# Kernel tuning notes

Measured on AMD Instinct MI355X. Metric: run time of the kernel, lower is better.

Reference implementation:

```python
import jax, jax.numpy as jnp
import numpy as np

B = 8192
NV = 778   # MANO vertices
NJ = 16    # LBS joints
PARENTS = np.array([0, 0, 1, 2, 0, 4, 5, 0, 7, 8, 0, 10, 11, 0, 13, 14])


def quat2mat(quat):
    # quat: [N,4] (w,x,y,z) -> [N,3,3]
    q = quat / jnp.linalg.norm(quat, axis=1, keepdims=True)
    w, x, y, z = q[:, 0], q[:, 1], q[:, 2], q[:, 3]
    w2, x2, y2, z2 = w * w, x * x, y * y, z * z
    wx, wy, wz = w * x, w * y, w * z
    xy, xz, yz = x * y, x * z, y * z
    R = jnp.stack([
        w2 + x2 - y2 - z2, 2 * xy - 2 * wz, 2 * wy + 2 * xz,
        2 * wz + 2 * xy, w2 - x2 + y2 - z2, 2 * yz - 2 * wx,
        2 * xz - 2 * wy, 2 * wx + 2 * yz, w2 - x2 - y2 + z2,
    ], axis=1)
    return R.reshape(-1, 3, 3)


def batch_rodrigues(theta):
    # theta: [N,3] axis-angle -> [N,3,3]
    angle = jnp.linalg.norm(theta + 1e-8, axis=1, keepdims=True)
    normalized = theta / angle
    half = angle * 0.5
    quat = jnp.concatenate([jnp.cos(half), jnp.sin(half) * normalized], axis=1)
    return quat2mat(quat)


def qmul(q, r):
    # Hamilton product, (w,x,y,z); q,r: [N,4]
    w1, x1, y1, z1 = q[:, 0], q[:, 1], q[:, 2], q[:, 3]
    w2, x2, y2, z2 = r[:, 0], r[:, 1], r[:, 2], r[:, 3]
    return jnp.stack([
        w1 * w2 - x1 * x2 - y1 * y2 - z1 * z2,
        w1 * x2 + x1 * w2 + y1 * z2 - z1 * y2,
        w1 * y2 - x1 * z2 + y1 * w2 + z1 * x2,
        w1 * z2 + x1 * y2 - y1 * x2 + z1 * w2,
    ], axis=1)


def make_A(R, t):
    # R: [B,J,3,3], t: [B,J,3] -> [B,J,4,4]
    Bn, J = R.shape[0], R.shape[1]
    top = jnp.concatenate([R, t[..., None]], axis=-1)              # [B,J,3,4]
    bot = jnp.broadcast_to(jnp.array([0., 0., 0., 1.], R.dtype), (Bn, J, 1, 4))
    return jnp.concatenate([top, bot], axis=-2)


def mano_forward(theta, delta_quat, user_shape, init_quat, init_trans,
                 v_template, shapedirs, J_regressor, posedirs, weights):
    Bn = theta.shape[0]
    beta = jnp.broadcast_to(user_shape, (Bn, user_shape.shape[-1]))
    v_shaped = (beta @ shapedirs).reshape(Bn, NV, 3) + v_template   # [B,778,3]
    J = jnp.einsum('bvc,vj->bjc', v_shaped, J_regressor)            # [B,21,3]

    Rs = batch_rodrigues(theta.reshape(-1, 3)).reshape(Bn, 15, 3, 3)
    pose_feature = (Rs - jnp.eye(3, dtype=Rs.dtype)).reshape(Bn, 135)
    v_posed = (pose_feature @ posedirs).reshape(Bn, NV, 3) + v_shaped

    quat = qmul(delta_quat, jnp.broadcast_to(init_quat, (Bn, 4)))
    root_R = quat2mat(quat)                                          # [B,3,3]
    Rs_all = jnp.concatenate([root_R[:, None], Rs], axis=1)          # [B,16,3,3]

    Jk = J[:, :NJ]                                                   # [B,16,3]
    rel = Jk - Jk[:, PARENTS]
    rel = rel.at[:, 0].set(Jk[:, 0])                                 # root keeps absolute pos
    A_local = make_A(Rs_all, rel)                                    # [B,16,4,4]

    # kinematic chain (fixed 16-joint tree)
    results = [A_local[:, 0]]
    for i in range(1, NJ):
        results.append(results[PARENTS[i]] @ A_local[:, i])
    G = jnp.stack(results, axis=1)                                   # [B,16,4,4]

    Jw0 = jnp.concatenate([Jk, jnp.zeros((Bn, NJ, 1), Jk.dtype)], axis=-1)
    init_bone = jnp.einsum('bjkl,bjl->bjk', G, Jw0)                  # [B,16,4]
    A = jnp.concatenate([G[..., :3], G[..., 3:] - init_bone[..., None]], axis=-1)

    T = jnp.einsum('vj,bjkl->bvkl', weights, A)                      # [B,778,4,4]
    vp_homo = jnp.concatenate([v_posed, jnp.ones((Bn, NV, 1), v_posed.dtype)], axis=-1)
    verts = jnp.einsum('bvkl,bvl->bvk', T, vp_homo)[..., :3]         # [B,778,3]

    joints = jnp.einsum('bvc,vj->bjc', verts, J_regressor)           # [B,21,3]
    trans = init_trans.reshape(Bn, 1, 3)
    return joints + trans  # get_skin=False path


def setup_inputs() -> dict:
    key = jax.random.key(0)
    ks = jax.random.split(key, 10)
    return {
        'theta': jax.random.normal(ks[0], (B, 45), jnp.float32) * 0.3,
        'delta_quat': jax.random.normal(ks[1], (B, 4), jnp.float32),
        'user_shape': jax.random.normal(ks[2], (1, 10), jnp.float32),
        'init_quat': jax.random.normal(ks[3], (1, 4), jnp.float32),
        'init_trans': jax.random.normal(ks[4], (B, 3), jnp.float32),
        'v_template': jax.random.normal(ks[5], (NV, 3), jnp.float32),
        'shapedirs': jax.random.normal(ks[6], (10, NV * 3), jnp.float32) * 0.01,
        'J_regressor': jax.random.uniform(ks[7], (NV, 21), jnp.float32) / NV,
        'posedirs': jax.random.normal(ks[8], (135, NV * 3), jnp.float32) * 0.01,
        'weights': jax.random.uniform(ks[9], (NV, NJ), jnp.float32),
    }


def reference(theta, delta_quat, user_shape, init_quat, init_trans,
              v_template, shapedirs, J_regressor, posedirs, weights):
    return mano_forward(theta, delta_quat, user_shape, init_quat, init_trans,
                        v_template, shapedirs, J_regressor, posedirs, weights)
```

## Files before the change

### kernel.cpp

```cpp
#include <hip/hip_runtime.h>
#include <math.h>

#define B_SIZE 8192
#define NVERT 778
#define NP 135
#define NEC 416
#define KS16 16

#define OFF_JK    0
#define OFF_C1    64
#define OFF_C0    400
#define OFF_P2    1408
#define OFF_PFT   137488
#define OFF_AT    1243408
#define OFF_PP_OVER 137488
#define OFF_PP_SAFE 2816272

__device__ inline void quat2mat_dev(float qw, float qx, float qy, float qz, float* R) {
  float n = sqrtf(qw*qw + qx*qx + qy*qy + qz*qz);
  float w = qw/n, x = qx/n, y = qy/n, z = qz/n;
  float w2=w*w, x2=x*x, y2=y*y, z2=z*z;
  float wx=w*x, wy=w*y, wz=w*z, xy=x*y, xz=x*z, yz=y*z;
  R[0]=w2+x2-y2-z2; R[1]=2.f*xy-2.f*wz; R[2]=2.f*wy+2.f*xz;
  R[3]=2.f*wz+2.f*xy; R[4]=w2-x2+y2-z2; R[5]=2.f*yz-2.f*wx;
  R[6]=2.f*xz-2.f*wy; R[7]=2.f*wx+2.f*yz; R[8]=w2-x2-y2+z2;
}

__device__ inline void rodrigues_dev(float tx, float ty, float tz, float* R) {
  float ax = tx + 1e-8f, ay = ty + 1e-8f, az = tz + 1e-8f;
  float angle = sqrtf(ax*ax + ay*ay + az*az);
  float nx = tx/angle, ny = ty/angle, nz = tz/angle;
  float half = 0.5f*angle;
  float cw = cosf(half), sw = sinf(half);
  quat2mat_dev(cw, sw*nx, sw*ny, sw*nz, R);
}

__device__ inline void pose_unit(const float* __restrict__ theta,
                                 const float* __restrict__ delta_quat,
                                 const float* __restrict__ init_quat,
                                 float* __restrict__ ws,
                                 const float* jk, const float* rel,
                                 int bb, int u, int lane) {
  int b = bb*256 + lane;
  float* pfT = ws + OFF_PFT;
  float* AT  = ws + OFF_AT;
  float w1=delta_quat[b*4+0], x1=delta_quat[b*4+1], y1=delta_quat[b*4+2], z1=delta_quat[b*4+3];
  float w2=init_quat[0], x2=init_quat[1], y2=init_quat[2], z2=init_quat[3];
  float qw = w1*w2 - x1*x2 - y1*y2 - z1*z2;
  float qx = w1*x2 + x1*w2 + y1*z2 - z1*y2;
  float qy = w1*y2 - x1*z2 + y1*w2 + z1*x2;
  float qz = w1*z2 + x1*y2 - y1*x2 + z1*w2;
  float G[12];
  quat2mat_dev(qw, qx, qy, qz, G);
  G[9] = rel[0]; G[10] = rel[1]; G[11] = rel[2];
  if (u == 5) {
    #pragma unroll
    for (int c = 0; c < 3; ++c) {
      float g0 = G[c*3+0], g1 = G[c*3+1], g2 = G[c*3+2];
      AT[(size_t)(c*4+0)*B_SIZE + b] = g0;
      AT[(size_t)(c*4+1)*B_SIZE + b] = g1;
      AT[(size_t)(c*4+2)*B_SIZE + b] = g2;
      AT[(size_t)(c*4+3)*B_SIZE + b] = G[9+c] - (g0*jk[0] + g1*jk[1] + g2*jk[2]);
    }
    return;
  }
  #pragma unroll
  for (int mstep = 0; mstep < 3; ++mstep) {
    int j = 3*u + 1 + mstep;
    int i = j - 1;
    float R[9];
    rodrigues_dev(theta[b*45+3*i+0], theta[b*45+3*i+1], theta[b*45+3*i+2], R);
    pfT[(size_t)(9*i+0)*B_SIZE + b] = R[0]-1.f;
    pfT[(size_t)(9*i+1)*B_SIZE + b] = R[1];
    pfT[(size_t)(9*i+2)*B_SIZE + b] = R[2];
    pfT[(size_t)(9*i+3)*B_SIZE + b] = R[3];
    pfT[(size_t)(9*i+4)*B_SIZE + b] = R[4]-1.f;
    pfT[(size_t)(9*i+5)*B_SIZE + b] = R[5];
    pfT[(size_t)(9*i+6)*B_SIZE + b] = R[6];
    pfT[(size_t)(9*i+7)*B_SIZE + b] = R[7];
    pfT[(size_t)(9*i+8)*B_SIZE + b] = R[8]-1.f;
    float nG[12];
    const float* rj = rel + j*3;
    #pragma unroll
    for (int r3 = 0; r3 < 3; ++r3) {
      float a0 = G[r3*3+0], a1 = G[r3*3+1], a2 = G[r3*3+2];
      nG[r3*3+0] = a0*R[0] + a1*R[3] + a2*R[6];
      nG[r3*3+1] = a0*R[1] + a1*R[4] + a2*R[7];
      nG[r3*3+2] = a0*R[2] + a1*R[5] + a2*R[8];
      nG[9+r3]   = G[9+r3] + a0*rj[0] + a1*rj[1] + a2*rj[2];
    }
    #pragma unroll
    for (int k = 0; k < 12; ++k) G[k] = nG[k];
    const float* jkj = jk + j*3;
    #pragma unroll
    for (int c = 0; c < 3; ++c) {
      float g0 = G[c*3+0], g1 = G[c*3+1], g2 = G[c*3+2];
      AT[(size_t)(j*12 + c*4+0)*B_SIZE + b] = g0;
      AT[(size_t)(j*12 + c*4+1)*B_SIZE + b] = g1;
      AT[(size_t)(j*12 + c*4+2)*B_SIZE + b] = g2;
      AT[(size_t)(j*12 + c*4+3)*B_SIZE + b] = G[9+c] - (g0*jkj[0] + g1*jkj[1] + g2*jkj[2]);
    }
  }
}

__device__ inline void kr_task(float* __restrict__ ws, int pp_off, int idx) {
  if (idx >= 416*84) return;
  int ec = idx / 84, q4 = idx - ec*84;
  const float* Pp = ws + pp_off;
  float4 s = make_float4(0.f, 0.f, 0.f, 0.f);
  #pragma unroll
  for (int ks = 0; ks < KS16; ++ks) {
    float4 v = *(const float4*)&Pp[(size_t)ks*NEC*336 + ec*336 + 4*q4];
    s.x += v.x; s.y += v.y; s.z += v.z; s.w += v.w;
  }
  float sv[4] = {s.x, s.y, s.z, s.w};
  #pragma unroll
  for (int r = 0; r < 4; ++r) {
    int q2 = 4*q4 + r;
    int jj2 = q2 >> 4, jj = q2 & 15;
    if (ec < 408) {
      int c = ec / 136, pp = ec - c*136;
      if (pp < 135) ws[OFF_P2 + (size_t)(jj2*135 + pp)*48 + jj*3 + c] = sv[r];
      else          ws[OFF_C0 + jj2*48 + jj*3 + c] = sv[r];
    } else if (ec == 408) {
      ws[OFF_C1 + jj2*16 + jj] = sv[r];
    }
  }
}

__global__ __launch_bounds__(256) void kA(const float* __restrict__ J_regressor,
                                          const float* __restrict__ weights,
                                          const float* __restrict__ posedirs,
                                          const float* __restrict__ user_shape,
                                          const float* __restrict__ v_template,
                                          const float* __restrict__ shapedirs,
                                          float* __restrict__ ws, int pp_off) {
  int tid = threadIdx.x;
  int bid = blockIdx.x;

  if (bid >= 416) {
    int j = bid - 416;
    __shared__ float red[3*256];
    __shared__ float ush[10];
    if (tid < 10) ush[tid] = user_shape[tid];
    __syncthreads();
    float p0 = 0.f, p1 = 0.f, p2 = 0.f;
    for (int v = tid; v < NVERT; v += 256) {
      float jr = J_regressor[v*21 + j];
      #pragma unroll
      for (int c = 0; c < 3; ++c) {
        int e = 3*v + c;
        float t = v_template[e];
        #pragma unroll
        for (int s = 0; s < 10; ++s) t += ush[s]*shapedirs[s*2334 + e];
        float val = jr * t;
        if (c == 0) p0 += val; else if (c == 1) p1 += val; else p2 += val;
      }
    }
    red[0*256+tid] = p0; red[1*256+tid] = p1; red[2*256+tid] = p2;
    __syncthreads();
    for (int s = 128; s > 0; s >>= 1) {
      if (tid < s) {
        red[0*256+tid] += red[0*256+tid+s];
        red[1*256+tid] += red[1*256+tid+s];
        red[2*256+tid] += red[2*256+tid+s];
      }
      __syncthreads();
    }
    if (tid < 3) ws[OFF_JK + j*3 + tid] = red[tid*256];
    return;
  }

  __shared__ float sJR[49*21];
  __shared__ float sW [49*16];
  __shared__ float sB [64*16];
  __shared__ float ush[10];
  if (tid < 10) ush[tid] = user_shape[tid];
  int ng = bid % 26;
  int ks = bid / 26;
  int vbeg = ks*49;
  int kt = min(NVERT - vbeg, 49);
  __syncthreads();
  for (int idx = tid; idx < kt*21; idx += 256) sJR[idx] = J_regressor[vbeg*21 + idx];
  for (int idx = tid; idx < kt*16; idx += 256) sW[idx]  = weights[vbeg*16 + idx];
  for (int idx = tid; idx < 16*64; idx += 256) {
    int s = idx >> 6, iv = idx & 63;
    if (iv < kt) {
      int ec = ng*16 + s;
      float val;
      if (ec > 408) val = 0.f;
      else if (ec == 408) val = 1.f;
      else {
        int c = ec / 136, pp = ec - c*136;
        int e = 3*(vbeg+iv) + c;
        if (pp == 135) {
          float t = v_template[e];
          #pragma unroll
          for (int s0 = 0; s0 < 10; ++s0) t += ush[s0]*shapedirs[s0*2334 + e];
          val = t;
        } else {
          val = posedirs[pp*2334 + e];
        }
      }
      sB[iv*16 + s] = val;
    }
  }
  __syncthreads();
  if (tid < 168) {
    int cg2 = (tid < 84) ? 0 : 1;
    int r4  = (tid < 84) ? tid : tid - 84;
    int q2 = 4*r4;
    int j2 = q2 >> 4;
    int jb = q2 & 15;
    float acc[4][8];
    #pragma unroll
    for (int r = 0; r < 4; ++r)
      #pragma unroll
      for (int s = 0; s < 8; ++s) acc[r][s] = 0.f;
    for (int i = 0; i < kt; ++i) {
      float jr = sJR[i*21 + j2];
      float4 w4 = *(const float4*)&sW[i*16 + jb];
      float4 b0 = *(const float4*)&sB[i*16 + cg2*8];
      float4 b1 = *(const float4*)&sB[i*16 + cg2*8 + 4];
      float wv[4] = {w4.x, w4.y, w4.z, w4.w};
      #pragma unroll
      for (int r = 0; r < 4; ++r) {
        float s2 = jr * wv[r];
        acc[r][0] += s2*b0.x; acc[r][1] += s2*b0.y;
        acc[r][2] += s2*b0.z; acc[r][3] += s2*b0.w;
        acc[r][4] += s2*b1.x; acc[r][5] += s2*b1.y;
        acc[r][6] += s2*b1.z; acc[r][7] += s2*b1.w;
      }
    }
    float* Pp = ws + pp_off + (size_t)ks*NEC*336;
    #pragma unroll
    for (int s = 0; s < 8; ++s) {
      int ec = ng*16 + cg2*8 + s;
      float4 v4 = make_float4(acc[0][s], acc[1][s], acc[2][s], acc[3][s]);
      *(float4*)&Pp[ec*336 + q2] = v4;
    }
  }
}

__global__ __launch_bounds__(256) void kRk4(const float* __restrict__ theta,
                                            const float* __restrict__ delta_quat,
                                            const float* __restrict__ init_quat,
                                            float* __restrict__ ws, int pp_off) {
  int bid = blockIdx.x;
  int tid = threadIdx.x;
  if (bid < 137) {
    kr_task(ws, pp_off, bid*256 + tid);
    return;
  }
  __shared__ float jk[48], rel[48];
  if (tid < 48) {
    float v = ws[OFF_JK + tid];
    jk[tid] = v;
    int j = tid/3, c = tid - j*3;
    float r;
    if (j == 0) r = v;
    else {
      int par = (((j-1) % 3) == 0) ? 0 : (j-1);
      r = v - ws[OFF_JK + par*3 + c];
    }
    rel[tid] = r;
  }
  __syncthreads();
  int s = bid & 7;
  int t = (bid - 137) >> 3;
  int bb = s + 8*(t & 3);
  int u  = t >> 2;
  pose_unit(theta, delta_quat, init_quat, ws, jk, rel, bb, u, tid);
}

__global__ void kR_fb(float* __restrict__ ws, int pp_off) {
  kr_task(ws, pp_off, blockIdx.x*256 + threadIdx.x);
}

__global__ __launch_bounds__(256) void k4_fb(const float* __restrict__ theta,
                                             const float* __restrict__ delta_quat,
                                             const float* __restrict__ init_quat,
                                             float* __restrict__ ws) {
  int bid = blockIdx.x;
  int tid = threadIdx.x;
  __shared__ float jk[48], rel[48];
  if (tid < 48) {
    float v = ws[OFF_JK + tid];
    jk[tid] = v;
    int j = tid/3, c = tid - j*3;
    float r;
    if (j == 0) r = v;
    else {
      int par = (((j-1) % 3) == 0) ? 0 : (j-1);
      r = v - ws[OFF_JK + par*3 + c];
    }
    rel[tid] = r;
  }
  __syncthreads();
  int s = bid & 7;
  int t = bid >> 3;
  int bb = s + 8*(t & 3);
  int u  = t >> 2;
  pose_unit(theta, delta_quat, init_quat, ws, jk, rel, bb, u, tid);
}

__global__ __launch_bounds__(256) void k5_main(const float* __restrict__ init_trans,
                                               const float* __restrict__ ws,
                                               float* __restrict__ out) {
  __shared__ int s_voff[1];
  int g = blockIdx.x;
  int xcd = g & 7, k = g >> 3;
  int br  = ((k & 3) << 3) | xcd;
  int j2  = k >> 2;
  int tid = threadIdx.x;
  int b   = br*256 + tid;

  if (tid == 0) s_voff[0] = j2*135*12;
  __syncthreads();
  int voff = s_voff[0];

  float4 acc[12];
  const float4* c04 = (const float4*)(ws + OFF_C0 + j2*48);
  #pragma unroll
  for (int i = 0; i < 12; ++i) acc[i] = c04[i];

  const float* pfT = ws + OFF_PFT;
  const float4* P24 = (const float4*)(ws + OFF_P2) + voff;
  #pragma unroll 3
  for (int p = 0; p < NP; ++p) {
    float pf = pfT[(size_t)p*B_SIZE + b];
    const float4* Pr = P24 + p*12;
    #pragma unroll
    for (int i = 0; i < 12; ++i) {
      float4 pv = Pr[i];
      acc[i].x += pf*pv.x; acc[i].y += pf*pv.y;
      acc[i].z += pf*pv.z; acc[i].w += pf*pv.w;
    }
  }

  float m[48];
  #pragma unroll
  for (int i = 0; i < 12; ++i) {
    m[4*i+0] = acc[i].x; m[4*i+1] = acc[i].y;
    m[4*i+2] = acc[i].z; m[4*i+3] = acc[i].w;
  }

  const float* AT  = ws + OFF_AT;
  const float* c1p = ws + OFF_C1 + j2*16;
  float o0 = 0.f, o1 = 0.f, o2 = 0.f;
  #pragma unroll
  for (int j = 0; j < 16; ++j) {
    float c1 = c1p[j];
    float m0 = m[3*j+0], m1 = m[3*j+1], m2 = m[3*j+2];
    #pragma unroll
    for (int k2 = 0; k2 < 3; ++k2) {
      float a0 = AT[(size_t)(j*12 + k2*4+0)*B_SIZE + b];
      float a1 = AT[(size_t)(j*12 + k2*4+1)*B_SIZE + b];
      float a2 = AT[(size_t)(j*12 + k2*4+2)*B_SIZE + b];
      float a3 = AT[(size_t)(j*12 + k2*4+3)*B_SIZE + b];
      float r = a0*m0 + a1*m1 + a2*m2 + a3*c1;
      if (k2 == 0) o0 += r; else if (k2 == 1) o1 += r; else o2 += r;
    }
  }
  size_t ob = ((size_t)b*21 + j2)*3;
  out[ob+0] = o0 + init_trans[b*3+0];
  out[ob+1] = o1 + init_trans[b*3+1];
  out[ob+2] = o2 + init_trans[b*3+2];
}

extern "C" void kernel_launch(void* const* d_in, const int* in_sizes, int n_in,
                              void* d_out, int out_size, void* d_ws, size_t ws_size,
                              hipStream_t stream) {
  const float* theta       = (const float*)d_in[0];
  const float* delta_quat  = (const float*)d_in[1];
  const float* user_shape  = (const float*)d_in[2];
  const float* init_quat   = (const float*)d_in[3];
  const float* init_trans  = (const float*)d_in[4];
  const float* v_template  = (const float*)d_in[5];
  const float* shapedirs   = (const float*)d_in[6];
  const float* J_regressor = (const float*)d_in[7];
  const float* posedirs    = (const float*)d_in[8];
  const float* weights     = (const float*)d_in[9];
  float* out = (float*)d_out;
  float* ws  = (float*)d_ws;

  size_t need = ((size_t)OFF_PP_SAFE + (size_t)KS16*NEC*336) * 4;
  if (ws_size >= need) {
    kA<<<432, 256, 0, stream>>>(J_regressor, weights, posedirs,
                                user_shape, v_template, shapedirs, ws, OFF_PP_SAFE);
    kRk4<<<329, 256, 0, stream>>>(theta, delta_quat, init_quat, ws, OFF_PP_SAFE);
  } else {
    kA<<<432, 256, 0, stream>>>(J_regressor, weights, posedirs,
                                user_shape, v_template, shapedirs, ws, OFF_PP_OVER);
    kR_fb<<<137, 256, 0, stream>>>(ws, OFF_PP_OVER);
    k4_fb<<<192, 256, 0, stream>>>(theta, delta_quat, init_quat, ws);
  }
  k5_main<<<672, 256, 0, stream>>>(init_trans, ws, out);
}
```

Before: 138.1 us.

## Replace split-K partial buffer and reduction pass with atomic accumulation

The split-K partial products used to be written to a large scratch buffer and summed by a separate reduction kernel. Now each split-K block atomically adds its results into the zeroed final P2/C0/C1 arrays. Zeroing is folded into the joint-regression kernel, and the pose/transform blocks are merged into the same launch as the GEMM blocks. This drops one launch and the partial-buffer round trip, at the cost of many scattered float atomics and non-deterministic summation order.

```diff
diff --git a/kernel.cpp b/kernel.cpp
--- a/kernel.cpp
+++ b/kernel.cpp
@@ -13,8 +13,7 @@
 #define OFF_P2    1408
 #define OFF_PFT   137488
 #define OFF_AT    1243408
-#define OFF_PP_OVER 137488
-#define OFF_PP_SAFE 2816272
+#define ZERO_N    137424
 
 __device__ inline void quat2mat_dev(float qw, float qx, float qy, float qz, float* R) {
   float n = sqrtf(qw*qw + qx*qx + qy*qy + qz*qz);
@@ -103,71 +102,83 @@
   }
 }
 
-__device__ inline void kr_task(float* __restrict__ ws, int pp_off, int idx) {
-  if (idx >= 416*84) return;
-  int ec = idx / 84, q4 = idx - ec*84;
-  const float* Pp = ws + pp_off;
-  float4 s = make_float4(0.f, 0.f, 0.f, 0.f);
-  #pragma unroll
-  for (int ks = 0; ks < KS16; ++ks) {
-    float4 v = *(const float4*)&Pp[(size_t)ks*NEC*336 + ec*336 + 4*q4];
-    s.x += v.x; s.y += v.y; s.z += v.z; s.w += v.w;
-  }
-  float sv[4] = {s.x, s.y, s.z, s.w};
-  #pragma unroll
-  for (int r = 0; r < 4; ++r) {
-    int q2 = 4*q4 + r;
-    int jj2 = q2 >> 4, jj = q2 & 15;
-    if (ec < 408) {
-      int c = ec / 136, pp = ec - c*136;
-      if (pp < 135) ws[OFF_P2 + (size_t)(jj2*135 + pp)*48 + jj*3 + c] = sv[r];
-      else          ws[OFF_C0 + jj2*48 + jj*3 + c] = sv[r];
-    } else if (ec == 408) {
-      ws[OFF_C1 + jj2*16 + jj] = sv[r];
-    }
-  }
-}
-
-__global__ __launch_bounds__(256) void kA(const float* __restrict__ J_regressor,
-                                          const float* __restrict__ weights,
-                                          const float* __restrict__ posedirs,
-                                          const float* __restrict__ user_shape,
-                                          const float* __restrict__ v_template,
-                                          const float* __restrict__ shapedirs,
-                                          float* __restrict__ ws, int pp_off) {
+__global__ __launch_bounds__(256) void kZJ(const float* __restrict__ J_regressor,
+                                           const float* __restrict__ user_shape,
+                                           const float* __restrict__ v_template,
+                                           const float* __restrict__ shapedirs,
+                                           float* __restrict__ ws) {
+  int bid = blockIdx.x;
   int tid = threadIdx.x;
+  if (bid < 537) {
+    int idx = bid*256 + tid;
+    if (idx < ZERO_N) ws[OFF_C1 + idx] = 0.f;
+    return;
+  }
+  int j = bid - 537;
+  __shared__ float red[3*256];
+  __shared__ float ush[10];
+  if (tid < 10) ush[tid] = user_shape[tid];
+  __syncthreads();
+  float p0 = 0.f, p1 = 0.f, p2 = 0.f;
+  for (int v = tid; v < NVERT; v += 256) {
+    float jr = J_regressor[v*21 + j];
+    #pragma unroll
+    for (int c = 0; c < 3; ++c) {
+      int e = 3*v + c;
+      float t = v_template[e];
+      #pragma unroll
+      for (int s = 0; s < 10; ++s) t += ush[s]*shapedirs[s*2334 + e];
+      float val = jr * t;
+      if (c == 0) p0 += val; else if (c == 1) p1 += val; else p2 += val;
+    }
+  }
+  red[0*256+tid] = p0; red[1*256+tid] = p1; red[2*256+tid] = p2;
+  __syncthreads();
+  for (int s = 128; s > 0; s >>= 1) {
+    if (tid < s) {
+      red[0*256+tid] += red[0*256+tid+s];
+      red[1*256+tid] += red[1*256+tid+s];
+      red[2*256+tid] += red[2*256+tid+s];
+    }
+    __syncthreads();
+  }
+  if (tid < 3) ws[OFF_JK + j*3 + tid] = red[tid*256];
+}
+
+__global__ __launch_bounds__(256) void kAP(const float* __restrict__ theta,
+                                           const float* __restrict__ delta_quat,
+                                           const float* __restrict__ init_quat,
+                                           const float* __restrict__ J_regressor,
+                                           const float* __restrict__ weights,
+                                           const float* __restrict__ posedirs,
+                                           const float* __restrict__ user_shape,
+                                           const float* __restrict__ v_template,
+                                           const float* __restrict__ shapedirs,
+                                           float* __restrict__ ws) {
   int bid = blockIdx.x;
+  int tid = threadIdx.x;
 
   if (bid >= 416) {
-    int j = bid - 416;
-    __shared__ float red[3*256];
-    __shared__ float ush[10];
-    if (tid < 10) ush[tid] = user_shape[tid];
+    __shared__ float jk[48], rel[48];
+    if (tid < 48) {
+      float v = ws[OFF_JK + tid];
+      jk[tid] = v;
+      int j = tid/3, c = tid - j*3;
+      float r;
+      if (j == 0) r = v;
+      else {
+        int par = (((j-1) % 3) == 0) ? 0 : (j-1);
+        r = v - ws[OFF_JK + par*3 + c];
+      }
+      rel[tid] = r;
+    }
     __syncthreads();
-    float p0 = 0.f, p1 = 0.f, p2 = 0.f;
-    for (int v = tid; v < NVERT; v += 256) {
-      float jr = J_regressor[v*21 + j];
-      #pragma unroll
-      for (int c = 0; c < 3; ++c) {
-        int e = 3*v + c;
-        float t = v_template[e];
-        #pragma unroll
-        for (int s = 0; s < 10; ++s) t += ush[s]*shapedirs[s*2334 + e];
-        float val = jr * t;
-        if (c == 0) p0 += val; else if (c == 1) p1 += val; else p2 += val;
-      }
-    }
-    red[0*256+tid] = p0; red[1*256+tid] = p1; red[2*256+tid] = p2;
-    __syncthreads();
-    for (int s = 128; s > 0; s >>= 1) {
-      if (tid < s) {
-        red[0*256+tid] += red[0*256+tid+s];
-        red[1*256+tid] += red[1*256+tid+s];
-        red[2*256+tid] += red[2*256+tid+s];
-      }
-      __syncthreads();
-    }
-    if (tid < 3) ws[OFF_JK + j*3 + tid] = red[tid*256];
+    int q = bid - 416;
+    int s = q & 7;
+    int t = q >> 3;
+    int bb = s + 8*(t & 3);
+    int u  = t >> 2;
+    pose_unit(theta, delta_quat, init_quat, ws, jk, rel, bb, u, tid);
     return;
   }
 
@@ -210,15 +221,16 @@
     int cg2 = (tid < 84) ? 0 : 1;
     int r4  = (tid < 84) ? tid : tid - 84;
     int q2 = 4*r4;
-    int j2 = q2 >> 4;
-    int jb = q2 & 15;
+    int j2b = q2 >> 4;
+    int jb  = q2 & 15;
+    (void)j2b;
     float acc[4][8];
     #pragma unroll
     for (int r = 0; r < 4; ++r)
       #pragma unroll
       for (int s = 0; s < 8; ++s) acc[r][s] = 0.f;
     for (int i = 0; i < kt; ++i) {
-      float jr = sJR[i*21 + j2];
+      float jr = sJR[i*21 + (q2 >> 4)];
       float4 w4 = *(const float4*)&sW[i*16 + jb];
       float4 b0 = *(const float4*)&sB[i*16 + cg2*8];
       float4 b1 = *(const float4*)&sB[i*16 + cg2*8 + 4];
@@ -232,76 +244,25 @@
         acc[r][6] += s2*b1.z; acc[r][7] += s2*b1.w;
       }
     }
-    float* Pp = ws + pp_off + (size_t)ks*NEC*336;
     #pragma unroll
     for (int s = 0; s < 8; ++s) {
       int ec = ng*16 + cg2*8 + s;
-      float4 v4 = make_float4(acc[0][s], acc[1][s], acc[2][s], acc[3][s]);
-      *(float4*)&Pp[ec*336 + q2] = v4;
-    }
-  }
-}
-
-__global__ __launch_bounds__(256) void kRk4(const float* __restrict__ theta,
-                                            const float* __restrict__ delta_quat,
-                                            const float* __restrict__ init_quat,
-                                            float* __restrict__ ws, int pp_off) {
-  int bid = blockIdx.x;
-  int tid = threadIdx.x;
-  if (bid < 137) {
-    kr_task(ws, pp_off, bid*256 + tid);
-    return;
-  }
-  __shared__ float jk[48], rel[48];
-  if (tid < 48) {
-    float v = ws[OFF_JK + tid];
-    jk[tid] = v;
-    int j = tid/3, c = tid - j*3;
-    float r;
-    if (j == 0) r = v;
-    else {
-      int par = (((j-1) % 3) == 0) ? 0 : (j-1);
-      r = v - ws[OFF_JK + par*3 + c];
-    }
-    rel[tid] = r;
-  }
-  __syncthreads();
-  int s = bid & 7;
-  int t = (bid - 137) >> 3;
-  int bb = s + 8*(t & 3);
-  int u  = t >> 2;
-  pose_unit(theta, delta_quat, init_quat, ws, jk, rel, bb, u, tid);
-}
-
-__global__ void kR_fb(float* __restrict__ ws, int pp_off) {
-  kr_task(ws, pp_off, blockIdx.x*256 + threadIdx.x);
-}
-
-__global__ __launch_bounds__(256) void k4_fb(const float* __restrict__ theta,
-                                             const float* __restrict__ delta_quat,
-                                             const float* __restrict__ init_quat,
-                                             float* __restrict__ ws) {
-  int bid = blockIdx.x;
-  int tid = threadIdx.x;
-  __shared__ float jk[48], rel[48];
-  if (tid < 48) {
-    float v = ws[OFF_JK + tid];
-    jk[tid] = v;
-    int j = tid/3, c = tid - j*3;
-    float r;
-    if (j == 0) r = v;
-    else {
-      int par = (((j-1) % 3) == 0) ? 0 : (j-1);
-      r = v - ws[OFF_JK + par*3 + c];
-    }
-    rel[tid] = r;
-  }
-  __syncthreads();
-  int s = bid & 7;
-  int t = bid >> 3;
-  int bb = s + 8*(t & 3);
-  int u  = t >> 2;
-  pose_unit(theta, delta_quat, init_quat, ws, jk, rel, bb, u, tid);
+      if (ec > 408) continue;
+      #pragma unroll
+      for (int r = 0; r < 4; ++r) {
+        int e = q2 + r;
+        int jj2 = e >> 4, jj = e & 15;
+        float val = acc[r][s];
+        if (ec == 408) {
+          atomicAdd(&ws[OFF_C1 + jj2*16 + jj], val);
+        } else {
+          int c = ec / 136, pp = ec - c*136;
+          if (pp < 135) atomicAdd(&ws[OFF_P2 + (size_t)(jj2*135 + pp)*48 + jj*3 + c], val);
+          else          atomicAdd(&ws[OFF_C0 + jj2*48 + jj*3 + c], val);
+        }
+      }
+    }
+  }
 }
 
 __global__ __launch_bounds__(256) void k5_main(const float* __restrict__ init_trans,
@@ -384,16 +345,9 @@
   float* out = (float*)d_out;
   float* ws  = (float*)d_ws;
 
-  size_t need = ((size_t)OFF_PP_SAFE + (size_t)KS16*NEC*336) * 4;
-  if (ws_size >= need) {
-    kA<<<432, 256, 0, stream>>>(J_regressor, weights, posedirs,
-                                user_shape, v_template, shapedirs, ws, OFF_PP_SAFE);
-    kRk4<<<329, 256, 0, stream>>>(theta, delta_quat, init_quat, ws, OFF_PP_SAFE);
-  } else {
-    kA<<<432, 256, 0, stream>>>(J_regressor, weights, posedirs,
-                                user_shape, v_template, shapedirs, ws, OFF_PP_OVER);
-    kR_fb<<<137, 256, 0, stream>>>(ws, OFF_PP_OVER);
-    k4_fb<<<192, 256, 0, stream>>>(theta, delta_quat, init_quat, ws);
-  }
+  kZJ<<<553, 256, 0, stream>>>(J_regressor, user_shape, v_template, shapedirs, ws);
+  kAP<<<608, 256, 0, stream>>>(theta, delta_quat, init_quat,
+                               J_regressor, weights, posedirs,
+                               user_shape, v_template, shapedirs, ws);
   k5_main<<<672, 256, 0, stream>>>(init_trans, ws, out);
 }
```

Result: slower. 222.8 us (+61.3%).

## Split k5 pose-blend and skinning work across thread pairs with shuffle reduction

Applied to the files above, without the earlier changes.

Each batch element in k5_main is now handled by two lanes instead of one. The lanes split the 135-term pose-feature loop in half, combine partial sums via __shfl_xor, then each lane skins half of the 16 joints before a final shuffle reduction. The grid doubles to 1344 blocks. The aim is more parallelism and latency hiding and a shorter per-thread dependency chain, at the cost of extra shuffles and a 48-float exchange. Each pf load now also covers only half the lanes, so coalescing gets worse.

```diff
diff --git a/kernel.cpp b/kernel.cpp
--- a/kernel.cpp
+++ b/kernel.cpp
@@ -310,24 +310,26 @@
   __shared__ int s_voff[1];
   int g = blockIdx.x;
   int xcd = g & 7, k = g >> 3;
-  int br  = ((k & 3) << 3) | xcd;
-  int j2  = k >> 2;
+  int br  = ((k & 7) << 3) | xcd;
+  int j2  = k >> 3;
   int tid = threadIdx.x;
-  int b   = br*256 + tid;
+  int h   = tid & 1;
+  int b   = br*128 + (tid >> 1);
 
   if (tid == 0) s_voff[0] = j2*135*12;
   __syncthreads();
   int voff = s_voff[0];
 
   float4 acc[12];
-  const float4* c04 = (const float4*)(ws + OFF_C0 + j2*48);
-  #pragma unroll
-  for (int i = 0; i < 12; ++i) acc[i] = c04[i];
+  #pragma unroll
+  for (int i = 0; i < 12; ++i) acc[i] = make_float4(0.f, 0.f, 0.f, 0.f);
 
   const float* pfT = ws + OFF_PFT;
   const float4* P24 = (const float4*)(ws + OFF_P2) + voff;
+  int pbeg = h ? 68 : 0;
+  int pend = h ? NP : 68;
   #pragma unroll 3
-  for (int p = 0; p < NP; ++p) {
+  for (int p = pbeg; p < pend; ++p) {
     float pf = pfT[(size_t)p*B_SIZE + b];
     const float4* Pr = P24 + p*12;
     #pragma unroll
@@ -344,28 +346,44 @@
     m[4*i+0] = acc[i].x; m[4*i+1] = acc[i].y;
     m[4*i+2] = acc[i].z; m[4*i+3] = acc[i].w;
   }
+  #pragma unroll
+  for (int i = 0; i < 48; ++i) m[i] += __shfl_xor(m[i], 1, 64);
+
+  float me[24];
+  #pragma unroll
+  for (int t = 0; t < 24; ++t) me[t] = h ? m[24 + t] : m[t];
+  const float* c0h = ws + OFF_C0 + j2*48 + 24*h;
+  #pragma unroll
+  for (int t = 0; t < 24; ++t) me[t] += c0h[t];
 
   const float* AT  = ws + OFF_AT;
-  const float* c1p = ws + OFF_C1 + j2*16;
+  const float* c1h = ws + OFF_C1 + j2*16 + 8*h;
+  int j12base = 96*h;
   float o0 = 0.f, o1 = 0.f, o2 = 0.f;
   #pragma unroll
-  for (int j = 0; j < 16; ++j) {
-    float c1 = c1p[j];
-    float m0 = m[3*j+0], m1 = m[3*j+1], m2 = m[3*j+2];
+  for (int jj = 0; jj < 8; ++jj) {
+    float c1 = c1h[jj];
+    float m0 = me[3*jj+0], m1 = me[3*jj+1], m2 = me[3*jj+2];
+    int jrow = j12base + jj*12;
     #pragma unroll
     for (int k2 = 0; k2 < 3; ++k2) {
-      float a0 = AT[(size_t)(j*12 + k2*4+0)*B_SIZE + b];
-      float a1 = AT[(size_t)(j*12 + k2*4+1)*B_SIZE + b];
-      float a2 = AT[(size_t)(j*12 + k2*4+2)*B_SIZE + b];
-      float a3 = AT[(size_t)(j*12 + k2*4+3)*B_SIZE + b];
+      float a0 = AT[(size_t)(jrow + k2*4+0)*B_SIZE + b];
+      float a1 = AT[(size_t)(jrow + k2*4+1)*B_SIZE + b];
+      float a2 = AT[(size_t)(jrow + k2*4+2)*B_SIZE + b];
+      float a3 = AT[(size_t)(jrow + k2*4+3)*B_SIZE + b];
       float r = a0*m0 + a1*m1 + a2*m2 + a3*c1;
       if (k2 == 0) o0 += r; else if (k2 == 1) o1 += r; else o2 += r;
     }
   }
-  size_t ob = ((size_t)b*21 + j2)*3;
-  out[ob+0] = o0 + init_trans[b*3+0];
-  out[ob+1] = o1 + init_trans[b*3+1];
-  out[ob+2] = o2 + init_trans[b*3+2];
+  o0 += __shfl_xor(o0, 1, 64);
+  o1 += __shfl_xor(o1, 1, 64);
+  o2 += __shfl_xor(o2, 1, 64);
+  if (h == 0) {
+    size_t ob = ((size_t)b*21 + j2)*3;
+    out[ob+0] = o0 + init_trans[b*3+0];
+    out[ob+1] = o1 + init_trans[b*3+1];
+    out[ob+2] = o2 + init_trans[b*3+2];
+  }
 }
 
 extern "C" void kernel_launch(void* const* d_in, const int* in_sizes, int n_in,
@@ -395,5 +413,5 @@
     kR_fb<<<137, 256, 0, stream>>>(ws, OFF_PP_OVER);
     k4_fb<<<192, 256, 0, stream>>>(theta, delta_quat, init_quat, ws);
   }
-  k5_main<<<672, 256, 0, stream>>>(init_trans, ws, out);
-}
+  k5_main<<<1344, 256, 0, stream>>>(init_trans, ws, out);
+}
```

New measurement: 324.6 us. 2.35x slower.

## Store A transforms as float4 interleaved and stage P2 weights in LDS

Applied to the files above, without the earlier changes.

The per-joint A matrix rows change from a planar float layout to a float4-interleaved layout, so each row is written and read with one 16-byte access per batch element instead of four scalar accesses. The main kernel now copies its 135x12 float4 slice of P2 into shared memory once per block and reads the pose loop operands from LDS instead of uniform global loads. This trades about 26 KB of LDS per block, which may limit occupancy, for fewer global and scalar memory transactions.

```diff
diff --git a/kernel.cpp b/kernel.cpp
--- a/kernel.cpp
+++ b/kernel.cpp
@@ -43,7 +43,7 @@
                                  int bb, int u, int lane) {
   int b = bb*256 + lane;
   float* pfT = ws + OFF_PFT;
-  float* AT  = ws + OFF_AT;
+  float4* AT4 = (float4*)(ws + OFF_AT);
   float w1=delta_quat[b*4+0], x1=delta_quat[b*4+1], y1=delta_quat[b*4+2], z1=delta_quat[b*4+3];
   float w2=init_quat[0], x2=init_quat[1], y2=init_quat[2], z2=init_quat[3];
   float qw = w1*w2 - x1*x2 - y1*y2 - z1*z2;
@@ -57,10 +57,8 @@
     #pragma unroll
     for (int c = 0; c < 3; ++c) {
       float g0 = G[c*3+0], g1 = G[c*3+1], g2 = G[c*3+2];
-      AT[(size_t)(c*4+0)*B_SIZE + b] = g0;
-      AT[(size_t)(c*4+1)*B_SIZE + b] = g1;
-      AT[(size_t)(c*4+2)*B_SIZE + b] = g2;
-      AT[(size_t)(c*4+3)*B_SIZE + b] = G[9+c] - (g0*jk[0] + g1*jk[1] + g2*jk[2]);
+      AT4[(size_t)(c)*B_SIZE + b] =
+        make_float4(g0, g1, g2, G[9+c] - (g0*jk[0] + g1*jk[1] + g2*jk[2]));
     }
     return;
   }
@@ -95,10 +93,8 @@
     #pragma unroll
     for (int c = 0; c < 3; ++c) {
       float g0 = G[c*3+0], g1 = G[c*3+1], g2 = G[c*3+2];
-      AT[(size_t)(j*12 + c*4+0)*B_SIZE + b] = g0;
-      AT[(size_t)(j*12 + c*4+1)*B_SIZE + b] = g1;
-      AT[(size_t)(j*12 + c*4+2)*B_SIZE + b] = g2;
-      AT[(size_t)(j*12 + c*4+3)*B_SIZE + b] = G[9+c] - (g0*jkj[0] + g1*jkj[1] + g2*jkj[2]);
+      AT4[(size_t)(j*3+c)*B_SIZE + b] =
+        make_float4(g0, g1, g2, G[9+c] - (g0*jkj[0] + g1*jkj[1] + g2*jkj[2]));
     }
   }
 }
@@ -307,7 +303,7 @@
 __global__ __launch_bounds__(256) void k5_main(const float* __restrict__ init_trans,
                                                const float* __restrict__ ws,
                                                float* __restrict__ out) {
-  __shared__ int s_voff[1];
+  __shared__ __align__(16) float4 sP2[NP*12];
   int g = blockIdx.x;
   int xcd = g & 7, k = g >> 3;
   int br  = ((k & 3) << 3) | xcd;
@@ -315,9 +311,9 @@
   int tid = threadIdx.x;
   int b   = br*256 + tid;
 
-  if (tid == 0) s_voff[0] = j2*135*12;
-  __syncthreads();
-  int voff = s_voff[0];
+  const float4* P2g = (const float4*)(ws + OFF_P2) + j2*NP*12;
+  for (int i = tid; i < NP*12; i += 256) sP2[i] = P2g[i];
+  __syncthreads();
 
   float4 acc[12];
   const float4* c04 = (const float4*)(ws + OFF_C0 + j2*48);
@@ -325,11 +321,10 @@
   for (int i = 0; i < 12; ++i) acc[i] = c04[i];
 
   const float* pfT = ws + OFF_PFT;
-  const float4* P24 = (const float4*)(ws + OFF_P2) + voff;
   #pragma unroll 3
   for (int p = 0; p < NP; ++p) {
     float pf = pfT[(size_t)p*B_SIZE + b];
-    const float4* Pr = P24 + p*12;
+    const float4* Pr = &sP2[p*12];
     #pragma unroll
     for (int i = 0; i < 12; ++i) {
       float4 pv = Pr[i];
@@ -345,7 +340,7 @@
     m[4*i+2] = acc[i].z; m[4*i+3] = acc[i].w;
   }
 
-  const float* AT  = ws + OFF_AT;
+  const float4* AT4 = (const float4*)(ws + OFF_AT);
   const float* c1p = ws + OFF_C1 + j2*16;
   float o0 = 0.f, o1 = 0.f, o2 = 0.f;
   #pragma unroll
@@ -354,11 +349,8 @@
     float m0 = m[3*j+0], m1 = m[3*j+1], m2 = m[3*j+2];
     #pragma unroll
     for (int k2 = 0; k2 < 3; ++k2) {
-      float a0 = AT[(size_t)(j*12 + k2*4+0)*B_SIZE + b];
-      float a1 = AT[(size_t)(j*12 + k2*4+1)*B_SIZE + b];
-      float a2 = AT[(size_t)(j*12 + k2*4+2)*B_SIZE + b];
-      float a3 = AT[(size_t)(j*12 + k2*4+3)*B_SIZE + b];
-      float r = a0*m0 + a1*m1 + a2*m2 + a3*c1;
+      float4 a = AT4[(size_t)(j*3+k2)*B_SIZE + b];
+      float r = a.x*m0 + a.y*m1 + a.z*m2 + a.w*c1;
       if (k2 == 0) o0 += r; else if (k2 == 1) o1 += r; else o2 += r;
     }
   }
```

Result: slower. 167.7 us (+21.5%).
